# Performance work log

Measured on AMD Instinct MI355X. Metric: run time of the kernel, lower is better.

The kernel has to match this reference:

```python
import jax, jax.numpy as jnp
import numpy as np

LN_EPS = 1e-5

def _layernorm(x, g, b):
    mu = jnp.mean(x, axis=-1, keepdims=True)
    var = jnp.mean((x - mu) ** 2, axis=-1, keepdims=True)
    return (x - mu) * jax.lax.rsqrt(var + LN_EPS) * g + b

def _mlp_ln(x, w1, b1, w2, b2, g, beta):
    h = jax.nn.silu(x @ w1 + b1)
    return _layernorm(h @ w2 + b2, g, beta)

def setup_inputs() -> dict:
    key = jax.random.key(0)
    ks = jax.random.split(key, 12)
    N, E, H = 50000, 600000, 128
    def lin(k, fan_in, fan_out):
        lim = 1.0 / np.sqrt(fan_in)
        kw, kb = jax.random.split(k)
        w = jax.random.uniform(kw, (fan_in, fan_out), jnp.float32, -lim, lim)
        b = jax.random.uniform(kb, (fan_out,), jnp.float32, -lim, lim)
        return w, b
    x = jax.random.normal(ks[0], (N, H), jnp.float32)
    edge_attr = jax.random.normal(ks[1], (E, H), jnp.float32)
    edge_index = jax.random.randint(ks[2], (2, E), 0, N, jnp.int64)
    eb_w1, eb_b1 = lin(ks[3], 3 * H, H)
    eb_w2, eb_b2 = lin(ks[4], H, H)
    nb_w1, nb_b1 = lin(ks[5], 2 * H, H)
    nb_w2, nb_b2 = lin(ks[6], H, H)
    return {
        'x': x, 'edge_attr': edge_attr, 'edge_index': edge_index,
        'eb_w1': eb_w1, 'eb_b1': eb_b1, 'eb_w2': eb_w2, 'eb_b2': eb_b2,
        'eb_g': jnp.ones((H,), jnp.float32), 'eb_beta': jnp.zeros((H,), jnp.float32),
        'nb_w1': nb_w1, 'nb_b1': nb_b1, 'nb_w2': nb_w2, 'nb_b2': nb_b2,
        'nb_g': jnp.ones((H,), jnp.float32), 'nb_beta': jnp.zeros((H,), jnp.float32),
    }

def reference(x, edge_attr, edge_index, eb_w1, eb_b1, eb_w2, eb_b2, eb_g, eb_beta,
              nb_w1, nb_b1, nb_w2, nb_b2, nb_g, nb_beta):
    src, dst = edge_index[0], edge_index[1]
    # Edge processor: gather src/dst node feats, concat with edge_attr, MLP+LN
    e_in = jnp.concatenate([x[src], x[dst], edge_attr], axis=-1)  # [E, 3H]
    e_new = _mlp_ln(e_in, eb_w1, eb_b1, eb_w2, eb_b2, eb_g, eb_beta)  # [E, H]
    # Node processor: scatter-add edge messages to receiver nodes, concat, MLP+LN
    agg = jax.ops.segment_sum(e_new, dst, num_segments=x.shape[0])  # [N, H]
    n_in = jnp.concatenate([x, agg], axis=-1)  # [N, 2H]
    x_new = _mlp_ln(n_in, nb_w1, nb_b1, nb_w2, nb_b2, nb_g, nb_beta)
    # Residuals
    return (x + x_new, edge_attr + e_new)
```

## Files before the change

kernel.cpp:

```cpp
#include <hip/hip_runtime.h>
#include <stdint.h>

typedef __bf16 bf16x8 __attribute__((ext_vector_type(8)));
typedef float f32x4 __attribute__((ext_vector_type(4)));
typedef unsigned short u16;

__device__ __forceinline__ u16 f2bf(float f) {
  uint32_t u = __float_as_uint(f);
  u += 0x7fffu + ((u >> 16) & 1u);
  return (u16)(u >> 16);
}
__device__ __forceinline__ float bf2f(u16 h) {
  return __uint_as_float(((uint32_t)h) << 16);
}
__device__ __forceinline__ ushort4 cvt4(float4 v) {
  return make_ushort4(f2bf(v.x), f2bf(v.y), f2bf(v.z), f2bf(v.w));
}

__device__ __forceinline__ f32x4 MFMA(bf16x8 a, bf16x8 b, f32x4 c) {
  return __builtin_amdgcn_mfma_f32_16x16x32_bf16(a, b, c, 0, 0, 0);
}

__global__ void pack_w_kernel(const float* __restrict__ W, u16* __restrict__ dst, int K) {
  int t = blockIdx.x * 256 + threadIdx.x;
  int total = (K >> 5) * 8 * 64;
  if (t >= total) return;
  int l = t & 63;
  int cf = (t >> 6) & 7;
  int ks = t >> 9;
  int kb = ks * 32 + ((l >> 4) << 3);
  int col = cf * 16 + (l & 15);
  u16 o[8];
#pragma unroll
  for (int j = 0; j < 8; ++j) o[j] = f2bf(W[(size_t)(kb + j) * 128 + col]);
  uint4 v;
  v.x = (uint32_t)o[0] | ((uint32_t)o[1] << 16);
  v.y = (uint32_t)o[2] | ((uint32_t)o[3] << 16);
  v.z = (uint32_t)o[4] | ((uint32_t)o[5] << 16);
  v.w = (uint32_t)o[6] | ((uint32_t)o[7] << 16);
  *(uint4*)(dst + (size_t)t * 8) = v;
}

__global__ void scan1_kernel(const int* __restrict__ cnt, int* __restrict__ bsum, int N) {
  const int b = blockIdx.x, t = threadIdx.x;
  const int lo = b * 2048 + t * 8;
  int s = 0;
#pragma unroll
  for (int i = 0; i < 8; ++i) {
    int idx = lo + i;
    if (idx < N) s += cnt[idx];
  }
  __shared__ int red[256];
  red[t] = s;
  __syncthreads();
  for (int off = 128; off; off >>= 1) {
    if (t < off) red[t] += red[t + off];
    __syncthreads();
  }
  if (t == 0) bsum[b] = red[0];
}

__global__ void scan2_kernel(int* __restrict__ bsum, int* __restrict__ roff, int NB, int N, int E) {
  __shared__ int p[512];
  const int t = threadIdx.x;
  p[t] = (t < NB) ? bsum[t] : 0;
  __syncthreads();
  for (int off = 1; off < 512; off <<= 1) {
    int v = (t >= off) ? p[t - off] : 0;
    __syncthreads();
    p[t] += v;
    __syncthreads();
  }
  if (t < NB) bsum[t] = (t == 0) ? 0 : p[t - 1];
  if (t == 0) roff[N] = E;
}

__global__ void scan3_kernel(const int* __restrict__ cnt, const int* __restrict__ bsum,
                             int* __restrict__ roff, int* __restrict__ cur, int N) {
  const int b = blockIdx.x, t = threadIdx.x;
  const int lo = b * 2048 + t * 8;
  int v[8];
  int s = 0;
#pragma unroll
  for (int i = 0; i < 8; ++i) {
    int idx = lo + i;
    v[i] = (idx < N) ? cnt[idx] : 0;
    s += v[i];
  }
  __shared__ int p[256];
  p[t] = s;
  __syncthreads();
  for (int off = 1; off < 256; off <<= 1) {
    int vv = (t >= off) ? p[t - off] : 0;
    __syncthreads();
    p[t] += vv;
    __syncthreads();
  }
  int base = bsum[b] + ((t == 0) ? 0 : p[t - 1]);
#pragma unroll
  for (int i = 0; i < 8; ++i) {
    int idx = lo + i;
    if (idx < N) {
      roff[idx] = base;
      cur[idx] = base;
      base += v[i];
    }
  }
}

__global__ void fill_kernel(const int* __restrict__ ei, int* __restrict__ cur,
                            int* __restrict__ elist, int E) {
  int e = blockIdx.x * 256 + threadIdx.x;
  if (e < E) {
    int p = atomicAdd(&cur[ei[E + e]], 1);
    elist[p] = e;
  }
}

__device__ __forceinline__ void stage_issue(const float4* __restrict__ src, int j, float4 v[8]) {
#pragma unroll
  for (int i = 0; i < 8; ++i) v[i] = src[j + 4 * i];
}
__device__ __forceinline__ void stage_zero(float4 v[8]) {
#pragma unroll
  for (int i = 0; i < 8; ++i) v[i] = make_float4(0.f, 0.f, 0.f, 0.f);
}
__device__ __forceinline__ void stage_write(u16* __restrict__ dst, int r, int j, const float4 v[8]) {
#pragma unroll
  for (int i = 0; i < 8; ++i) *(ushort4*)(dst + r * 136 + (j + 4 * i) * 4) = cvt4(v[i]);
}

template <int ASTRIDE>
__device__ __forceinline__ void gemm4(const u16* __restrict__ abase, const u16* __restrict__ pw,
                                      int ksbase, int w, int lane, f32x4 acc[4][2]) {
#pragma unroll
  for (int ks = 0; ks < 4; ++ks) {
    bf16x8 b0 = *(const bf16x8*)(pw + ((size_t)((ksbase + ks) * 8 + w * 2 + 0) * 64 + lane) * 8);
    bf16x8 b1 = *(const bf16x8*)(pw + ((size_t)((ksbase + ks) * 8 + w * 2 + 1) * 64 + lane) * 8);
#pragma unroll
    for (int rf = 0; rf < 4; ++rf) {
      bf16x8 a = *(const bf16x8*)(abase + rf * (16 * ASTRIDE) + ks * 32);
      acc[rf][0] = MFMA(a, b0, acc[rf][0]);
      acc[rf][1] = MFMA(a, b1, acc[rf][1]);
    }
  }
}

template <int MODE>
__global__ __launch_bounds__(256, 4) void edge_kernel(
    const float* __restrict__ x, const float* __restrict__ edge_attr,
    const int* __restrict__ ei,
    const u16* __restrict__ pw1, const u16* __restrict__ pw2,
    const float* __restrict__ b1, const float* __restrict__ b2,
    const float* __restrict__ gln, const float* __restrict__ bln,
    float* __restrict__ out_edge, float* __restrict__ agg,
    float* __restrict__ emsg, int* __restrict__ cnt, int E) {
  alignas(16) __shared__ u16 sLds[2 * 64 * 136];
  u16* buf0 = sLds;
  u16* buf1 = sLds + 64 * 136;
  float* sY = (float*)sLds;

  const int tid = threadIdx.x;
  const int w = tid >> 6;
  const int lane = tid & 63;
  const int eBase = blockIdx.x * 64;
  const int r = tid >> 2, j = tid & 3;
  const int e0 = eBase + r;
  const bool ev = (e0 < E);
  const int e = ev ? e0 : 0;
  const int s = ei[e];
  const int d = ei[E + e];

  if (MODE >= 1 && ev && j == 0) atomicAdd(&cnt[d], 1);

  const u16* a0 = buf0 + (lane & 15) * 136 + ((lane >> 4) << 3);
  const u16* a1 = buf1 + (lane & 15) * 136 + ((lane >> 4) << 3);

  float4 v[8];

  if (ev) stage_issue((const float4*)(x + (size_t)s * 128), j, v); else stage_zero(v);
  stage_write(buf0, r, j, v);
  __syncthreads();

  f32x4 acc[4][2];
#pragma unroll
  for (int rf = 0; rf < 4; ++rf)
#pragma unroll
    for (int cf = 0; cf < 2; ++cf) acc[rf][cf] = 0.f;

  if (ev) stage_issue((const float4*)(x + (size_t)d * 128), j, v); else stage_zero(v);
  gemm4<136>(a0, pw1, 0, w, lane, acc);
  stage_write(buf1, r, j, v);
  __syncthreads();

  if (ev) stage_issue((const float4*)(edge_attr + (size_t)e * 128), j, v); else stage_zero(v);
  gemm4<136>(a1, pw1, 4, w, lane, acc);
  stage_write(buf0, r, j, v);
  __syncthreads();

  gemm4<136>(a0, pw1, 8, w, lane, acc);
  {
    const int colb = w * 32;
#pragma unroll
    for (int cf = 0; cf < 2; ++cf) {
      const int col = colb + cf * 16 + (lane & 15);
      const float bias = b1[col];
#pragma unroll
      for (int rf = 0; rf < 4; ++rf) {
#pragma unroll
        for (int jj = 0; jj < 4; ++jj) {
          const int row = rf * 16 + ((lane >> 4) << 2) + jj;
          float vv = acc[rf][cf][jj] + bias;
          float h = vv / (1.f + __expf(-vv));
          buf1[row * 136 + col] = f2bf(h);
        }
      }
    }
  }
  __syncthreads();

  f32x4 acc2[4][2];
#pragma unroll
  for (int rf = 0; rf < 4; ++rf)
#pragma unroll
    for (int cf = 0; cf < 2; ++cf) acc2[rf][cf] = 0.f;
  gemm4<136>(a1, pw2, 0, w, lane, acc2);
  float ea[32];
#pragma unroll
  for (int i = 0; i < 32; ++i) ea[i] = bf2f(buf0[r * 136 + j + 4 * i]);
  __syncthreads();

  {
    const int colb = w * 32;
#pragma unroll
    for (int cf = 0; cf < 2; ++cf) {
      const int col = colb + cf * 16 + (lane & 15);
      const float bias = b2[col];
#pragma unroll
      for (int rf = 0; rf < 4; ++rf) {
#pragma unroll
        for (int jj = 0; jj < 4; ++jj) {
          const int row = rf * 16 + ((lane >> 4) << 2) + jj;
          sY[row * 132 + col] = acc2[rf][cf][jj] + bias;
        }
      }
    }
  }
  __syncthreads();

  if (ev) {
    float vals[32];
    float sum = 0.f, sq = 0.f;
#pragma unroll
    for (int i = 0; i < 32; ++i) {
      float vv = sY[r * 132 + j + i * 4];
      vals[i] = vv;
      sum += vv;
      sq += vv * vv;
    }
    sum += __shfl_xor(sum, 1);
    sum += __shfl_xor(sum, 2);
    sq += __shfl_xor(sq, 1);
    sq += __shfl_xor(sq, 2);
    const float mu = sum * (1.f / 128.f);
    const float rs = rsqrtf(sq * (1.f / 128.f) - mu * mu + 1e-5f);
    float* orow = out_edge + (size_t)e * 128;
    float* emrow = emsg + (size_t)e * 128;
    float* aggrow = agg + (size_t)d * 128;
#pragma unroll
    for (int i = 0; i < 32; ++i) {
      const int c = j + i * 4;
      const float o = (vals[i] - mu) * rs * gln[c] + bln[c];
      orow[c] = ea[i] + o;
      if (MODE == 2) emrow[c] = o;
      if (MODE == 0) atomicAdd(aggrow + c, o);
    }
  }
}

template <int MODE>
__global__ __launch_bounds__(256, 4) void node_kernel(
    const float* __restrict__ x, const float* __restrict__ aggin,
    const int* __restrict__ roff, const int* __restrict__ elist,
    const float* __restrict__ emsg,
    const float* __restrict__ out_edge_ro, const float* __restrict__ edge_attr,
    const u16* __restrict__ pw1, const u16* __restrict__ pw2,
    const float* __restrict__ b1, const float* __restrict__ b2,
    const float* __restrict__ gln, const float* __restrict__ bln,
    float* __restrict__ outx, int N) {
  alignas(16) __shared__ u16 sN[64 * 392];
  float* sY = (float*)sN;

  const int tid = threadIdx.x;
  const int w = tid >> 6;
  const int lane = tid & 63;
  const int nBase = blockIdx.x * 64;
  const int r = tid >> 2, j = tid & 3;
  const int n0 = nBase + r;
  const bool nv = (n0 < N);
  const int n = nv ? n0 : 0;

  {
    float4 v[8];
    if (nv) stage_issue((const float4*)(x + (size_t)n * 128), j, v); else stage_zero(v);
#pragma unroll
    for (int i = 0; i < 8; ++i) *(ushort4*)(sN + r * 392 + (j + 4 * i) * 4) = cvt4(v[i]);
    if (MODE == 0) {
      if (nv) stage_issue((const float4*)(aggin + (size_t)n * 128), j, v); else stage_zero(v);
#pragma unroll
      for (int i = 0; i < 8; ++i) {
        ushort4 h4 = cvt4(v[i]);
        float4 lo4 = make_float4(v[i].x - bf2f(h4.x), v[i].y - bf2f(h4.y),
                                 v[i].z - bf2f(h4.z), v[i].w - bf2f(h4.w));
        *(ushort4*)(sN + r * 392 + 128 + (j + 4 * i) * 4) = h4;
        *(ushort4*)(sN + r * 392 + 256 + (j + 4 * i) * 4) = cvt4(lo4);
      }
    } else {
      float a[32];
#pragma unroll
      for (int i = 0; i < 32; ++i) a[i] = 0.f;
      if (nv) {
        const int k0 = roff[n];
        const int k1 = roff[n + 1];
        if (MODE == 2) {
          const float* base = emsg + 32 * j;
          for (int k = k0; k < k1; ++k) {
            const int eid = elist[k];
            const float4* p = (const float4*)(base + (size_t)eid * 128);
#pragma unroll
            for (int q = 0; q < 8; ++q) {
              float4 ov = p[q];
              a[4 * q + 0] += ov.x;
              a[4 * q + 1] += ov.y;
              a[4 * q + 2] += ov.z;
              a[4 * q + 3] += ov.w;
            }
          }
        } else {
          for (int k = k0; k < k1; ++k) {
            const int eid = elist[k];
            const float4* po = (const float4*)(out_edge_ro + (size_t)eid * 128 + 32 * j);
            const float4* pa = (const float4*)(edge_attr + (size_t)eid * 128 + 32 * j);
#pragma unroll
            for (int q = 0; q < 8; ++q) {
              float4 ov = po[q], av = pa[q];
              a[4 * q + 0] += ov.x - av.x;
              a[4 * q + 1] += ov.y - av.y;
              a[4 * q + 2] += ov.z - av.z;
              a[4 * q + 3] += ov.w - av.w;
            }
          }
        }
      }
#pragma unroll
      for (int t = 0; t < 8; ++t) {
        ushort4 h4, l4;
#pragma unroll
        for (int q = 0; q < 4; ++q) {
          const float av = a[4 * t + q];
          const u16 hb = f2bf(av);
          const float lv = av - bf2f(hb);
          ((u16*)&h4)[q] = hb;
          ((u16*)&l4)[q] = f2bf(lv);
        }
        *(ushort4*)(sN + r * 392 + 128 + 32 * j + 4 * t) = h4;
        *(ushort4*)(sN + r * 392 + 256 + 32 * j + 4 * t) = l4;
      }
    }
  }
  __syncthreads();

  f32x4 acc[4][2];
#pragma unroll
  for (int rf = 0; rf < 4; ++rf)
#pragma unroll
    for (int cf = 0; cf < 2; ++cf) acc[rf][cf] = 0.f;
  {
    const u16* abase = sN + (lane & 15) * 392 + ((lane >> 4) << 3);
    gemm4<392>(abase, pw1, 0, w, lane, acc);
    gemm4<392>(abase + 128, pw1, 4, w, lane, acc);
    gemm4<392>(abase + 256, pw1, 4, w, lane, acc);
  }
  __syncthreads();

  {
    const int colb = w * 32;
#pragma unroll
    for (int cf = 0; cf < 2; ++cf) {
      const int col = colb + cf * 16 + (lane & 15);
      const float bias = b1[col];
#pragma unroll
      for (int rf = 0; rf < 4; ++rf) {
#pragma unroll
        for (int jj = 0; jj < 4; ++jj) {
          const int row = rf * 16 + ((lane >> 4) << 2) + jj;
          float vv = acc[rf][cf][jj] + bias;
          float h = vv / (1.f + __expf(-vv));
          sN[row * 136 + col] = f2bf(h);
        }
      }
    }
  }
  __syncthreads();

  f32x4 acc2[4][2];
#pragma unroll
  for (int rf = 0; rf < 4; ++rf)
#pragma unroll
    for (int cf = 0; cf < 2; ++cf) acc2[rf][cf] = 0.f;
  {
    const u16* abase = sN + (lane & 15) * 136 + ((lane >> 4) << 3);
    gemm4<136>(abase, pw2, 0, w, lane, acc2);
  }
  __syncthreads();

  {
    const int colb = w * 32;
#pragma unroll
    for (int cf = 0; cf < 2; ++cf) {
      const int col = colb + cf * 16 + (lane & 15);
      const float bias = b2[col];
#pragma unroll
      for (int rf = 0; rf < 4; ++rf) {
#pragma unroll
        for (int jj = 0; jj < 4; ++jj) {
          const int row = rf * 16 + ((lane >> 4) << 2) + jj;
          sY[row * 133 + col] = acc2[rf][cf][jj] + bias;
        }
      }
    }
  }
  __syncthreads();

  if (nv) {
    const int cb = 32 * j;
    float vals[32];
    float sum = 0.f, sq = 0.f;
#pragma unroll
    for (int i = 0; i < 32; ++i) {
      float vv = sY[r * 133 + cb + i];
      vals[i] = vv;
      sum += vv;
      sq += vv * vv;
    }
    sum += __shfl_xor(sum, 1);
    sum += __shfl_xor(sum, 2);
    sq += __shfl_xor(sq, 1);
    sq += __shfl_xor(sq, 2);
    const float mu = sum * (1.f / 128.f);
    const float rs = rsqrtf(sq * (1.f / 128.f) - mu * mu + 1e-5f);
    const float* xrow = x + (size_t)n * 128 + cb;
    float* orow = outx + (size_t)n * 128 + cb;
#pragma unroll
    for (int q = 0; q < 8; ++q) {
      float4 xv = *(const float4*)(xrow + 4 * q);
      float4 t4;
      t4.x = xv.x + (vals[4 * q + 0] - mu) * rs * gln[cb + 4 * q + 0] + bln[cb + 4 * q + 0];
      t4.y = xv.y + (vals[4 * q + 1] - mu) * rs * gln[cb + 4 * q + 1] + bln[cb + 4 * q + 1];
      t4.z = xv.z + (vals[4 * q + 2] - mu) * rs * gln[cb + 4 * q + 2] + bln[cb + 4 * q + 2];
      t4.w = xv.w + (vals[4 * q + 3] - mu) * rs * gln[cb + 4 * q + 3] + bln[cb + 4 * q + 3];
      *(float4*)(orow + 4 * q) = t4;
    }
  }
}

extern "C" void kernel_launch(void* const* d_in, const int* in_sizes, int n_in,
                              void* d_out, int out_size, void* d_ws, size_t ws_size,
                              hipStream_t stream) {
  const float* x = (const float*)d_in[0];
  const float* edge_attr = (const float*)d_in[1];
  const int* ei = (const int*)d_in[2];
  const float* eb_w1 = (const float*)d_in[3];
  const float* eb_b1 = (const float*)d_in[4];
  const float* eb_w2 = (const float*)d_in[5];
  const float* eb_b2 = (const float*)d_in[6];
  const float* eb_g = (const float*)d_in[7];
  const float* eb_beta = (const float*)d_in[8];
  const float* nb_w1 = (const float*)d_in[9];
  const float* nb_b1 = (const float*)d_in[10];
  const float* nb_w2 = (const float*)d_in[11];
  const float* nb_b2 = (const float*)d_in[12];
  const float* nb_g = (const float*)d_in[13];
  const float* nb_beta = (const float*)d_in[14];

  const int N = in_sizes[0] / 128;
  const int E = in_sizes[1] / 128;

  float* out = (float*)d_out;
  float* agg = out;
  float* out_edge = out + (size_t)N * 128;

  u16* pw1e = (u16*)d_ws;
  u16* pw2e = pw1e + 384 * 128;
  u16* pw1n = pw2e + 128 * 128;
  u16* pw2n = pw1n + 256 * 128;
  const size_t w_bytes = (size_t)(384 + 128 + 256 + 128) * 128 * 2;
  int* cnt = (int*)((char*)d_ws + w_bytes);
  int* roff = cnt + N;
  int* cur = roff + N + 1;
  int* elist = cur + N;
  int* bsum = elist + E;
  const size_t csr_bytes = (size_t)4 * (3 * (size_t)N + 1 + (size_t)E + 512);
  size_t em_off = w_bytes + csr_bytes;
  em_off = (em_off + 15) & ~(size_t)15;
  float* emsg = (float*)((char*)d_ws + em_off);
  const size_t need_emsg = em_off + (size_t)E * 128 * 4;
  const size_t need_csr = w_bytes + csr_bytes;
  const int mode = (ws_size >= need_emsg) ? 2 : ((ws_size >= need_csr) ? 1 : 0);

  pack_w_kernel<<<(384 * 16 + 255) / 256, 256, 0, stream>>>(eb_w1, pw1e, 384);
  pack_w_kernel<<<(128 * 16 + 255) / 256, 256, 0, stream>>>(eb_w2, pw2e, 128);
  pack_w_kernel<<<(256 * 16 + 255) / 256, 256, 0, stream>>>(nb_w1, pw1n, 256);
  pack_w_kernel<<<(128 * 16 + 255) / 256, 256, 0, stream>>>(nb_w2, pw2n, 128);

  const int eg = (E + 63) / 64, ng = (N + 63) / 64;
  const int NB = (N + 2047) / 2048;

  if (mode >= 1) {
    hipMemsetAsync(cnt, 0, (size_t)N * 4, stream);
    if (mode == 2) {
      edge_kernel<2><<<eg, 256, 0, stream>>>(x, edge_attr, ei, pw1e, pw2e, eb_b1, eb_b2,
                                             eb_g, eb_beta, out_edge, agg, emsg, cnt, E);
    } else {
      edge_kernel<1><<<eg, 256, 0, stream>>>(x, edge_attr, ei, pw1e, pw2e, eb_b1, eb_b2,
                                             eb_g, eb_beta, out_edge, agg, emsg, cnt, E);
    }
    scan1_kernel<<<NB, 256, 0, stream>>>(cnt, bsum, N);
    scan2_kernel<<<1, 512, 0, stream>>>(bsum, roff, NB, N, E);
    scan3_kernel<<<NB, 256, 0, stream>>>(cnt, bsum, roff, cur, N);
    fill_kernel<<<(E + 255) / 256, 256, 0, stream>>>(ei, cur, elist, E);
    if (mode == 2) {
      node_kernel<2><<<ng, 256, 0, stream>>>(x, nullptr, roff, elist, emsg, nullptr, nullptr,
                                             pw1n, pw2n, nb_b1, nb_b2, nb_g, nb_beta, out, N);
    } else {
      node_kernel<1><<<ng, 256, 0, stream>>>(x, nullptr, roff, elist, nullptr, out_edge,
                                             edge_attr, pw1n, pw2n, nb_b1, nb_b2, nb_g,
                                             nb_beta, out, N);
    }
  } else {
    hipMemsetAsync(agg, 0, (size_t)N * 128 * sizeof(float), stream);
    edge_kernel<0><<<eg, 256, 0, stream>>>(x, edge_attr, ei, pw1e, pw2e, eb_b1, eb_b2,
                                           eb_g, eb_beta, out_edge, agg, emsg, cnt, E);
    node_kernel<0><<<ng, 256, 0, stream>>>(x, agg, nullptr, nullptr, nullptr, nullptr,
                                           nullptr, pw1n, pw2n, nb_b1, nb_b2, nb_g,
                                           nb_beta, out, N);
  }
}
```

Baseline: 531.3 us.

## Process edges in destination-sorted order so node aggregation reads messages contiguously

In the default mode, CSR construction now runs before the edge kernel through a separate count kernel. The edge kernel then processes edges in destination-sorted order via elist and writes each message to emsg at its sorted position. The node kernel can then sum contiguous emsg rows instead of gathering them by edge id. The cost is random gathers of x[src] and edge_attr plus scattered out_edge writes in the edge kernel, where before only the x gathers were random, along with one extra launch.

```diff
diff --git a/kernel.cpp b/kernel.cpp
--- a/kernel.cpp
+++ b/kernel.cpp
@@ -41,6 +41,11 @@
   *(uint4*)(dst + (size_t)t * 8) = v;
 }
 
+__global__ void count_kernel(const int* __restrict__ ei, int* __restrict__ cnt, int E) {
+  int e = blockIdx.x * 256 + threadIdx.x;
+  if (e < E) atomicAdd(&cnt[ei[E + e]], 1);
+}
+
 __global__ void scan1_kernel(const int* __restrict__ cnt, int* __restrict__ bsum, int N) {
   const int b = blockIdx.x, t = threadIdx.x;
   const int lo = b * 2048 + t * 8;
@@ -130,15 +135,15 @@
   for (int i = 0; i < 8; ++i) *(ushort4*)(dst + r * 136 + (j + 4 * i) * 4) = cvt4(v[i]);
 }
 
-template <int ASTRIDE>
+template <int ASTRIDE, int NRF>
 __device__ __forceinline__ void gemm4(const u16* __restrict__ abase, const u16* __restrict__ pw,
-                                      int ksbase, int w, int lane, f32x4 acc[4][2]) {
+                                      int ksbase, int w, int lane, f32x4 acc[NRF][2]) {
 #pragma unroll
   for (int ks = 0; ks < 4; ++ks) {
     bf16x8 b0 = *(const bf16x8*)(pw + ((size_t)((ksbase + ks) * 8 + w * 2 + 0) * 64 + lane) * 8);
     bf16x8 b1 = *(const bf16x8*)(pw + ((size_t)((ksbase + ks) * 8 + w * 2 + 1) * 64 + lane) * 8);
 #pragma unroll
-    for (int rf = 0; rf < 4; ++rf) {
+    for (int rf = 0; rf < NRF; ++rf) {
       bf16x8 a = *(const bf16x8*)(abase + rf * (16 * ASTRIDE) + ks * 32);
       acc[rf][0] = MFMA(a, b0, acc[rf][0]);
       acc[rf][1] = MFMA(a, b1, acc[rf][1]);
@@ -149,7 +154,7 @@
 template <int MODE>
 __global__ __launch_bounds__(256, 4) void edge_kernel(
     const float* __restrict__ x, const float* __restrict__ edge_attr,
-    const int* __restrict__ ei,
+    const int* __restrict__ ei, const int* __restrict__ elist,
     const u16* __restrict__ pw1, const u16* __restrict__ pw2,
     const float* __restrict__ b1, const float* __restrict__ b2,
     const float* __restrict__ gln, const float* __restrict__ bln,
@@ -165,13 +170,13 @@
   const int lane = tid & 63;
   const int eBase = blockIdx.x * 64;
   const int r = tid >> 2, j = tid & 3;
-  const int e0 = eBase + r;
-  const bool ev = (e0 < E);
-  const int e = ev ? e0 : 0;
+  const int kpos = eBase + r;
+  const bool ev = (kpos < E);
+  const int e = ev ? ((MODE == 2) ? elist[kpos] : kpos) : 0;
   const int s = ei[e];
   const int d = ei[E + e];
 
-  if (MODE >= 1 && ev && j == 0) atomicAdd(&cnt[d], 1);
+  if (MODE == 1 && ev && j == 0) atomicAdd(&cnt[d], 1);
 
   const u16* a0 = buf0 + (lane & 15) * 136 + ((lane >> 4) << 3);
   const u16* a1 = buf1 + (lane & 15) * 136 + ((lane >> 4) << 3);
@@ -189,16 +194,16 @@
     for (int cf = 0; cf < 2; ++cf) acc[rf][cf] = 0.f;
 
   if (ev) stage_issue((const float4*)(x + (size_t)d * 128), j, v); else stage_zero(v);
-  gemm4<136>(a0, pw1, 0, w, lane, acc);
+  gemm4<136, 4>(a0, pw1, 0, w, lane, acc);
   stage_write(buf1, r, j, v);
   __syncthreads();
 
   if (ev) stage_issue((const float4*)(edge_attr + (size_t)e * 128), j, v); else stage_zero(v);
-  gemm4<136>(a1, pw1, 4, w, lane, acc);
+  gemm4<136, 4>(a1, pw1, 4, w, lane, acc);
   stage_write(buf0, r, j, v);
   __syncthreads();
 
-  gemm4<136>(a0, pw1, 8, w, lane, acc);
+  gemm4<136, 4>(a0, pw1, 8, w, lane, acc);
   {
     const int colb = w * 32;
 #pragma unroll
@@ -224,7 +229,7 @@
   for (int rf = 0; rf < 4; ++rf)
 #pragma unroll
     for (int cf = 0; cf < 2; ++cf) acc2[rf][cf] = 0.f;
-  gemm4<136>(a1, pw2, 0, w, lane, acc2);
+  gemm4<136, 4>(a1, pw2, 0, w, lane, acc2);
   float ea[32];
 #pragma unroll
   for (int i = 0; i < 32; ++i) ea[i] = bf2f(buf0[r * 136 + j + 4 * i]);
@@ -265,7 +270,7 @@
     const float mu = sum * (1.f / 128.f);
     const float rs = rsqrtf(sq * (1.f / 128.f) - mu * mu + 1e-5f);
     float* orow = out_edge + (size_t)e * 128;
-    float* emrow = emsg + (size_t)e * 128;
+    float* emrow = emsg + (size_t)kpos * 128;
     float* aggrow = agg + (size_t)d * 128;
 #pragma unroll
     for (int i = 0; i < 32; ++i) {
@@ -323,17 +328,15 @@
         const int k0 = roff[n];
         const int k1 = roff[n + 1];
         if (MODE == 2) {
-          const float* base = emsg + 32 * j;
           for (int k = k0; k < k1; ++k) {
-            const int eid = elist[k];
-            const float4* p = (const float4*)(base + (size_t)eid * 128);
-#pragma unroll
-            for (int q = 0; q < 8; ++q) {
-              float4 ov = p[q];
-              a[4 * q + 0] += ov.x;
-              a[4 * q + 1] += ov.y;
-              a[4 * q + 2] += ov.z;
-              a[4 * q + 3] += ov.w;
+            const float4* p = (const float4*)(emsg + (size_t)k * 128 + 32 * j);
+#pragma unroll
+            for (int qq = 0; qq < 8; ++qq) {
+              float4 ov = p[qq];
+              a[4 * qq + 0] += ov.x;
+              a[4 * qq + 1] += ov.y;
+              a[4 * qq + 2] += ov.z;
+              a[4 * qq + 3] += ov.w;
             }
           }
         } else {
@@ -342,12 +345,12 @@
             const float4* po = (const float4*)(out_edge_ro + (size_t)eid * 128 + 32 * j);
             const float4* pa = (const float4*)(edge_attr + (size_t)eid * 128 + 32 * j);
 #pragma unroll
-            for (int q = 0; q < 8; ++q) {
-              float4 ov = po[q], av = pa[q];
-              a[4 * q + 0] += ov.x - av.x;
-              a[4 * q + 1] += ov.y - av.y;
-              a[4 * q + 2] += ov.z - av.z;
-              a[4 * q + 3] += ov.w - av.w;
+            for (int qq = 0; qq < 8; ++qq) {
+              float4 ov = po[qq], av = pa[qq];
+              a[4 * qq + 0] += ov.x - av.x;
+              a[4 * qq + 1] += ov.y - av.y;
+              a[4 * qq + 2] += ov.z - av.z;
+              a[4 * qq + 3] += ov.w - av.w;
             }
           }
         }
@@ -356,12 +359,12 @@
       for (int t = 0; t < 8; ++t) {
         ushort4 h4, l4;
 #pragma unroll
-        for (int q = 0; q < 4; ++q) {
-          const float av = a[4 * t + q];
+        for (int qq = 0; qq < 4; ++qq) {
+          const float av = a[4 * t + qq];
           const u16 hb = f2bf(av);
           const float lv = av - bf2f(hb);
-          ((u16*)&h4)[q] = hb;
-          ((u16*)&l4)[q] = f2bf(lv);
+          ((u16*)&h4)[qq] = hb;
+          ((u16*)&l4)[qq] = f2bf(lv);
         }
         *(ushort4*)(sN + r * 392 + 128 + 32 * j + 4 * t) = h4;
         *(ushort4*)(sN + r * 392 + 256 + 32 * j + 4 * t) = l4;
@@ -377,9 +380,9 @@
     for (int cf = 0; cf < 2; ++cf) acc[rf][cf] = 0.f;
   {
     const u16* abase = sN + (lane & 15) * 392 + ((lane >> 4) << 3);
-    gemm4<392>(abase, pw1, 0, w, lane, acc);
-    gemm4<392>(abase + 128, pw1, 4, w, lane, acc);
-    gemm4<392>(abase + 256, pw1, 4, w, lane, acc);
+    gemm4<392, 4>(abase, pw1, 0, w, lane, acc);
+    gemm4<392, 4>(abase + 128, pw1, 4, w, lane, acc);
+    gemm4<392, 4>(abase + 256, pw1, 4, w, lane, acc);
   }
   __syncthreads();
 
@@ -410,7 +413,7 @@
     for (int cf = 0; cf < 2; ++cf) acc2[rf][cf] = 0.f;
   {
     const u16* abase = sN + (lane & 15) * 136 + ((lane >> 4) << 3);
-    gemm4<136>(abase, pw2, 0, w, lane, acc2);
+    gemm4<136, 4>(abase, pw2, 0, w, lane, acc2);
   }
   __syncthreads();
 
@@ -452,14 +455,14 @@
     const float* xrow = x + (size_t)n * 128 + cb;
     float* orow = outx + (size_t)n * 128 + cb;
 #pragma unroll
-    for (int q = 0; q < 8; ++q) {
-      float4 xv = *(const float4*)(xrow + 4 * q);
+    for (int qq = 0; qq < 8; ++qq) {
+      float4 xv = *(const float4*)(xrow + 4 * qq);
       float4 t4;
-      t4.x = xv.x + (vals[4 * q + 0] - mu) * rs * gln[cb + 4 * q + 0] + bln[cb + 4 * q + 0];
-      t4.y = xv.y + (vals[4 * q + 1] - mu) * rs * gln[cb + 4 * q + 1] + bln[cb + 4 * q + 1];
-      t4.z = xv.z + (vals[4 * q + 2] - mu) * rs * gln[cb + 4 * q + 2] + bln[cb + 4 * q + 2];
-      t4.w = xv.w + (vals[4 * q + 3] - mu) * rs * gln[cb + 4 * q + 3] + bln[cb + 4 * q + 3];
-      *(float4*)(orow + 4 * q) = t4;
+      t4.x = xv.x + (vals[4 * qq + 0] - mu) * rs * gln[cb + 4 * qq + 0] + bln[cb + 4 * qq + 0];
+      t4.y = xv.y + (vals[4 * qq + 1] - mu) * rs * gln[cb + 4 * qq + 1] + bln[cb + 4 * qq + 1];
+      t4.z = xv.z + (vals[4 * qq + 2] - mu) * rs * gln[cb + 4 * qq + 2] + bln[cb + 4 * qq + 2];
+      t4.w = xv.w + (vals[4 * qq + 3] - mu) * rs * gln[cb + 4 * qq + 3] + bln[cb + 4 * qq + 3];
+      *(float4*)(orow + 4 * qq) = t4;
     }
   }
 }
@@ -516,31 +519,32 @@
   const int eg = (E + 63) / 64, ng = (N + 63) / 64;
   const int NB = (N + 2047) / 2048;
 
-  if (mode >= 1) {
+  if (mode == 2) {
     hipMemsetAsync(cnt, 0, (size_t)N * 4, stream);
-    if (mode == 2) {
-      edge_kernel<2><<<eg, 256, 0, stream>>>(x, edge_attr, ei, pw1e, pw2e, eb_b1, eb_b2,
-                                             eb_g, eb_beta, out_edge, agg, emsg, cnt, E);
-    } else {
-      edge_kernel<1><<<eg, 256, 0, stream>>>(x, edge_attr, ei, pw1e, pw2e, eb_b1, eb_b2,
-                                             eb_g, eb_beta, out_edge, agg, emsg, cnt, E);
-    }
+    count_kernel<<<(E + 255) / 256, 256, 0, stream>>>(ei, cnt, E);
     scan1_kernel<<<NB, 256, 0, stream>>>(cnt, bsum, N);
     scan2_kernel<<<1, 512, 0, stream>>>(bsum, roff, NB, N, E);
     scan3_kernel<<<NB, 256, 0, stream>>>(cnt, bsum, roff, cur, N);
     fill_kernel<<<(E + 255) / 256, 256, 0, stream>>>(ei, cur, elist, E);
-    if (mode == 2) {
-      node_kernel<2><<<ng, 256, 0, stream>>>(x, nullptr, roff, elist, emsg, nullptr, nullptr,
-                                             pw1n, pw2n, nb_b1, nb_b2, nb_g, nb_beta, out, N);
-    } else {
-      node_kernel<1><<<ng, 256, 0, stream>>>(x, nullptr, roff, elist, nullptr, out_edge,
-                                             edge_attr, pw1n, pw2n, nb_b1, nb_b2, nb_g,
-                                             nb_beta, out, N);
-    }
+    edge_kernel<2><<<eg, 256, 0, stream>>>(x, edge_attr, ei, elist, pw1e, pw2e, eb_b1,
+                                           eb_b2, eb_g, eb_beta, out_edge, agg, emsg, cnt, E);
+    node_kernel<2><<<ng, 256, 0, stream>>>(x, nullptr, roff, elist, emsg, nullptr, nullptr,
+                                           pw1n, pw2n, nb_b1, nb_b2, nb_g, nb_beta, out, N);
+  } else if (mode == 1) {
+    hipMemsetAsync(cnt, 0, (size_t)N * 4, stream);
+    edge_kernel<1><<<eg, 256, 0, stream>>>(x, edge_attr, ei, nullptr, pw1e, pw2e, eb_b1,
+                                           eb_b2, eb_g, eb_beta, out_edge, agg, emsg, cnt, E);
+    scan1_kernel<<<NB, 256, 0, stream>>>(cnt, bsum, N);
+    scan2_kernel<<<1, 512, 0, stream>>>(bsum, roff, NB, N, E);
+    scan3_kernel<<<NB, 256, 0, stream>>>(cnt, bsum, roff, cur, N);
+    fill_kernel<<<(E + 255) / 256, 256, 0, stream>>>(ei, cur, elist, E);
+    node_kernel<1><<<ng, 256, 0, stream>>>(x, nullptr, roff, elist, nullptr, out_edge,
+                                           edge_attr, pw1n, pw2n, nb_b1, nb_b2, nb_g,
+                                           nb_beta, out, N);
   } else {
     hipMemsetAsync(agg, 0, (size_t)N * 128 * sizeof(float), stream);
-    edge_kernel<0><<<eg, 256, 0, stream>>>(x, edge_attr, ei, pw1e, pw2e, eb_b1, eb_b2,
-                                           eb_g, eb_beta, out_edge, agg, emsg, cnt, E);
+    edge_kernel<0><<<eg, 256, 0, stream>>>(x, edge_attr, ei, nullptr, pw1e, pw2e, eb_b1,
+                                           eb_b2, eb_g, eb_beta, out_edge, agg, emsg, cnt, E);
     node_kernel<0><<<ng, 256, 0, stream>>>(x, agg, nullptr, nullptr, nullptr, nullptr,
                                            nullptr, pw1n, pw2n, nb_b1, nb_b2, nb_g,
                                            nb_beta, out, N);
```

New measurement: 553.0 us. +4.1%, slower.
